# Kernel tuning notes

Measured on AMD Instinct MI355X. Metric: run time of the kernel, lower is better.

The kernel has to match this reference:

```python
import jax, jax.numpy as jnp
import numpy as np
from jax import lax

BN_EPS = 1e-5

def conv_bn_prelu(x, w, b, scale, bias, a):
    # Conv2d(k=3, pad=1, stride=1) in NCHW / OIHW layout
    y = lax.conv_general_dilated(x, w, window_strides=(1, 1), padding='SAME',
                                 dimension_numbers=('NCHW', 'OIHW', 'NCHW'))
    y = y + b[None, :, None, None]
    # BatchNorm2d, training-mode batch statistics over (B, H, W)
    mean = jnp.mean(y, axis=(0, 2, 3), keepdims=True)
    var = jnp.var(y, axis=(0, 2, 3), keepdims=True)
    y = (y - mean) * lax.rsqrt(var + BN_EPS)
    y = y * scale[None, :, None, None] + bias[None, :, None, None]
    # PReLU with single shared slope parameter
    return jnp.where(y >= 0, y, a * y)

def setup_inputs() -> dict:
    key = jax.random.key(0)
    ks = jax.random.split(key, 7)
    B, C, H, W = 4, 64, 64, 64
    x = jax.random.normal(ks[0], (B, C, H, W), dtype=jnp.float32)
    conv_w = jax.random.normal(ks[1], (C, C, 3, 3), dtype=jnp.float32) * 0.05
    conv_b = jax.random.normal(ks[2], (C,), dtype=jnp.float32) * 0.05
    bn_scale = jax.random.uniform(ks[3], (C,), dtype=jnp.float32, minval=0.5, maxval=1.5)
    bn_bias = jax.random.normal(ks[4], (C,), dtype=jnp.float32) * 0.05
    prelu_a = jnp.full((1,), 0.25, dtype=jnp.float32)
    gamma = jax.random.normal(ks[5], (1,), dtype=jnp.float32)
    return {'x': x, 'conv_w': conv_w, 'conv_b': conv_b, 'bn_scale': bn_scale,
            'bn_bias': bn_bias, 'prelu_a': prelu_a, 'gamma': gamma}

def reference(x, conv_w, conv_b, bn_scale, bn_bias, prelu_a, gamma):
    B, C, H, W = x.shape
    N = H * W
    feat = conv_bn_prelu(x, conv_w, conv_b, bn_scale, bn_bias, prelu_a)  # (B,C,H,W)
    f = feat.reshape(B, C, N)  # proj_query = f^T, proj_key = f, proj_value = f
    # energy[b,i,j] = sum_c f[b,c,i] * f[b,c,j]  -> (B, N, N)
    energy = jnp.einsum('bci,bcj->bij', f, f)
    # energy_new = rowmax - energy, softmax over last dim
    energy_new = jnp.max(energy, axis=-1, keepdims=True) - energy
    attn = jax.nn.softmax(energy_new, axis=-1)
    # out = bmm(proj_value, attention^T): out[b,c,i] = sum_j f[b,c,j] * attn[b,i,j]
    out = jnp.einsum('bcj,bij->bci', f, attn).reshape(B, C, H, W)
    return gamma * out + feat
```

## Files before the change

kernel.cpp:

```cpp
#include <hip/hip_runtime.h>

constexpr int kB = 4, kC = 64, kH = 64, kW = 64, kN = kH * kW;
constexpr float kEps = 1e-5f;
constexpr int SPLIT = 4;

typedef __attribute__((ext_vector_type(8))) short short8;
typedef __attribute__((ext_vector_type(4))) float f32x4;
typedef unsigned short u16;

__device__ inline unsigned pkbf(float a, float b) {
  unsigned ua = __float_as_uint(a), ub = __float_as_uint(b);
  ua += 0x7fff + ((ua >> 16) & 1);
  ub += 0x7fff + ((ub >> 16) & 1);
  return (ua >> 16) | (ub & 0xffff0000u);
}

__global__ __launch_bounds__(256) void prep_w_kernel(const float* __restrict__ w,
                                                     u16* __restrict__ wA) {
  int idx = blockIdx.x * 256 + threadIdx.x;
  if (idx < 64 * 576) {
    int oc = idx / 576, r = idx - oc * 576;
    int khw = r >> 6, ic = r & 63;
    float v = w[(oc * 64 + ic) * 9 + khw];
    unsigned u = __float_as_uint(v);
    u += 0x7fff + ((u >> 16) & 1);
    wA[idx] = (u16)(u >> 16);
  }
}

__global__ __launch_bounds__(256) void conv_kernel(const float* __restrict__ x,
                                                   const u16* __restrict__ wA,
                                                   const float* __restrict__ bias,
                                                   float* __restrict__ y) {
  const int tid = threadIdx.x;
  const int lane = tid & 63;
  const int wv = tid >> 6;
  const int bx = blockIdx.x;
  const int b = bx >> 7;
  const int h = (bx & 127) >> 1;
  const int w0 = (bx & 1) * 32;
  const int lw = lane & 15, lg = lane >> 4;

  __shared__ __align__(16) u16 xt[3 * 40 * 64];

#pragma unroll
  for (int rep = 0; rep < 4; ++rep) {
    int idx = rep * 256 + tid;
    if (idx < 960) {
      int kh = idx / 320;
      int t = idx - kh * 320;
      int gw = t >> 5, icp = t & 31;
      int wb = w0 - 4 + gw * 4;
      int hh = h + kh - 1;
      float4 va = {0.f, 0.f, 0.f, 0.f}, vb = {0.f, 0.f, 0.f, 0.f};
      if (hh >= 0 && hh < 64 && wb >= 0 && wb < 64) {
        va = *(const float4*)&x[((b * 64 + icp * 2) * 64 + hh) * 64 + wb];
        vb = *(const float4*)&x[((b * 64 + icp * 2 + 1) * 64 + hh) * 64 + wb];
      }
      float av[4] = {va.x, va.y, va.z, va.w};
      float bv[4] = {vb.x, vb.y, vb.z, vb.w};
#pragma unroll
      for (int j = 0; j < 4; ++j) {
        int wc = gw * 4 + j;
        *(unsigned*)&xt[(kh * 40 + wc) * 64 + (((icp >> 2) ^ (wc & 7)) * 8 + (icp & 3) * 2)] =
            pkbf(av[j], bv[j]);
      }
    }
  }
  __syncthreads();

  const int oc0 = wv * 16;
  short8 af[18];
#pragma unroll
  for (int kc = 0; kc < 18; ++kc)
    af[kc] = *(const short8*)&wA[(oc0 + lw) * 576 + kc * 32 + lg * 8];

  f32x4 acc[2];
  acc[0] = (f32x4){0.f, 0.f, 0.f, 0.f};
  acc[1] = (f32x4){0.f, 0.f, 0.f, 0.f};
#pragma unroll
  for (int kc = 0; kc < 18; ++kc) {
    const int khw = kc >> 1;
    const int kh = khw / 3, kwv = khw % 3;
#pragma unroll
    for (int nt = 0; nt < 2; ++nt) {
      int wc = nt * 16 + lw + kwv + 3;
      short8 bf = *(const short8*)&xt[(kh * 40 + wc) * 64 + ((((kc & 1) * 4 + lg) ^ (wc & 7)) * 8)];
      acc[nt] = __builtin_amdgcn_mfma_f32_16x16x32_bf16(af[kc], bf, acc[nt], 0, 0, 0);
    }
  }
#pragma unroll
  for (int nt = 0; nt < 2; ++nt)
#pragma unroll
    for (int r = 0; r < 4; ++r) {
      int oc = oc0 + lg * 4 + r;
      y[((b * 64 + oc) * 64 + h) * 64 + w0 + nt * 16 + lw] = acc[nt][r] + bias[oc];
    }
}

__global__ __launch_bounds__(256) void stats_kernel(const float* __restrict__ y,
                                                    const float* __restrict__ scale,
                                                    const float* __restrict__ bias,
                                                    float* __restrict__ AB) {
  const int c = blockIdx.x;
  const int tid = threadIdx.x;
  float s = 0.f, s2 = 0.f;
  for (int b = 0; b < kB; ++b) {
    const float* p = y + (b * kC + c) * kN;
    for (int i = tid * 4; i < kN; i += 1024) {
      float4 v = *(const float4*)(p + i);
      s += v.x + v.y + v.z + v.w;
      s2 += v.x * v.x + v.y * v.y + v.z * v.z + v.w * v.w;
    }
  }
  __shared__ float rs[256], rq[256];
  rs[tid] = s;
  rq[tid] = s2;
  __syncthreads();
  for (int off = 128; off > 0; off >>= 1) {
    if (tid < off) { rs[tid] += rs[tid + off]; rq[tid] += rq[tid + off]; }
    __syncthreads();
  }
  if (tid == 0) {
    const float inv_n = 1.f / (float)(kB * kN);
    float mean = rs[0] * inv_n;
    float var = rq[0] * inv_n - mean * mean;
    float A = scale[c] * rsqrtf(var + kEps);
    AB[c] = A;
    AB[kC + c] = bias[c] - mean * A;
  }
}

__global__ __launch_bounds__(256) void pack_kernel(const float* __restrict__ y,
                                                   const float* __restrict__ AB,
                                                   const float* __restrict__ pa,
                                                   float* __restrict__ feat,
                                                   u16* __restrict__ fbfA,
                                                   u16* __restrict__ fbfB) {
  __shared__ float ls[64 * 65];
  const int tid = threadIdx.x;
  const int b = blockIdx.x >> 6;
  const int n0 = (blockIdx.x & 63) << 6;
  {
    const int c = tid >> 2, nj = (tid & 3) << 4;
    const float A = AB[c], Bc = AB[kC + c], a = pa[0];
    const float* yp = y + ((b * kC + c) * kN) + n0 + nj;
    float f[16];
#pragma unroll
    for (int v = 0; v < 4; ++v) {
      float4 xv = *(const float4*)(yp + v * 4);
      float t;
      t = fmaf(A, xv.x, Bc); f[v * 4 + 0] = t >= 0.f ? t : a * t;
      t = fmaf(A, xv.y, Bc); f[v * 4 + 1] = t >= 0.f ? t : a * t;
      t = fmaf(A, xv.z, Bc); f[v * 4 + 2] = t >= 0.f ? t : a * t;
      t = fmaf(A, xv.w, Bc); f[v * 4 + 3] = t >= 0.f ? t : a * t;
    }
    float* fo = feat + ((b * kC + c) * kN) + n0 + nj;
#pragma unroll
    for (int v = 0; v < 4; ++v) {
      float4 fv = {f[v * 4 + 0], f[v * 4 + 1], f[v * 4 + 2], f[v * 4 + 3]};
      *(float4*)(fo + v * 4) = fv;
    }
#pragma unroll
    for (int v = 0; v < 16; ++v) ls[c * 65 + nj + v] = f[v];
  }
  __syncthreads();
  {
    int chunk = tid >> 5, pt = chunk >> 1, kc = chunk & 1;
    int lp2 = (tid & 31) * 2;
    u16* dst = fbfA + ((size_t)((b * 256 + (n0 >> 4) + pt) * 2 + kc)) * 512;
#pragma unroll
    for (int e = 0; e < 2; ++e) {
      int L = lp2 + e;
      int n = pt * 16 + (L & 15);
      int cb = kc * 32 + (L >> 4) * 8;
      float v[8];
#pragma unroll
      for (int r = 0; r < 8; ++r) v[r] = ls[(cb + r) * 65 + n];
      uint4 o = {pkbf(v[0], v[1]), pkbf(v[2], v[3]), pkbf(v[4], v[5]), pkbf(v[6], v[7])};
      *(uint4*)&dst[L * 8] = o;
    }
  }
  {
    int chunk = tid >> 5, jt = chunk >> 2, ct = chunk & 3;
    int lp2 = (tid & 31) * 2;
    u16* dst = fbfB + ((size_t)((b * 128 + (n0 >> 5) + jt) * 4 + ct)) * 512;
#pragma unroll
    for (int e = 0; e < 2; ++e) {
      int L = lp2 + e;
      int c = ct * 16 + (L & 15);
      int nb = jt * 32 + (L >> 4) * 8;
      float v[8];
#pragma unroll
      for (int r = 0; r < 8; ++r) v[r] = ls[c * 65 + nb + r];
      uint4 o = {pkbf(v[0], v[1]), pkbf(v[2], v[3]), pkbf(v[4], v[5]), pkbf(v[6], v[7])};
      *(uint4*)&dst[L * 8] = o;
    }
  }
}

__global__ __launch_bounds__(256, 2) void attn_kernel(const u16* __restrict__ fbfA,
                                                      const u16* __restrict__ fbfB,
                                                      float* __restrict__ Op,
                                                      float* __restrict__ lp) {
  const int tid = threadIdx.x;
  const int lane = tid & 63;
  const int w = tid >> 6;
  const int bx = blockIdx.x;
  const int s = bx & 3, itb = (bx >> 2) & 15, b = bx >> 6;
  const int c15 = lane & 15, g = lane >> 4;

  __shared__ __align__(16) u16 Ps[4][64 * 40];
  u16* ps = &Ps[w][0];
  const int pw_off = c15 * 40 + g * 4;
  const int pr_off = c15 * 40 + g * 8;

  const uint4* fA = (const uint4*)fbfA;
  const uint4* fB = (const uint4*)fbfB;

  uint4 qf[4][2];
  const int ptq = itb * 16 + w * 4;
#pragma unroll
  for (int it = 0; it < 4; ++it)
#pragma unroll
    for (int kc = 0; kc < 2; ++kc) {
      uint4 q = fA[(size_t)((b * 256 + ptq + it) * 2 + kc) * 64 + lane];
      q.x ^= 0x80008000u; q.y ^= 0x80008000u; q.z ^= 0x80008000u; q.w ^= 0x80008000u;
      qf[it][kc] = q;
    }

  const short8 ones = {0x3F80, 0x3F80, 0x3F80, 0x3F80, 0x3F80, 0x3F80, 0x3F80, 0x3F80};

  f32x4 oacc[4][4];
  f32x4 lacc[4];
#pragma unroll
  for (int it = 0; it < 4; ++it) {
    lacc[it] = (f32x4){0.f, 0.f, 0.f, 0.f};
#pragma unroll
    for (int ct = 0; ct < 4; ++ct) oacc[it][ct] = (f32x4){0.f, 0.f, 0.f, 0.f};
  }

#pragma unroll 2
  for (int jj = 0; jj < 32; ++jj) {
    const int j0 = (s * 32 + jj) * 32;
    const int ca = (b * 256 + (j0 >> 4)) * 2;
    uint4 a00 = fA[(size_t)(ca + 0) * 64 + lane];
    uint4 a01 = fA[(size_t)(ca + 1) * 64 + lane];
    uint4 a10 = fA[(size_t)(ca + 2) * 64 + lane];
    uint4 a11 = fA[(size_t)(ca + 3) * 64 + lane];
    const int cb = (b * 128 + (j0 >> 5)) * 4;
    uint4 v0 = fB[(size_t)(cb + 0) * 64 + lane];
    uint4 v1 = fB[(size_t)(cb + 1) * 64 + lane];
    uint4 v2 = fB[(size_t)(cb + 2) * 64 + lane];
    uint4 v3 = fB[(size_t)(cb + 3) * 64 + lane];

    f32x4 sv[2][4];
#pragma unroll
    for (int it = 0; it < 4; ++it) {
      f32x4 z0 = (f32x4){0.f, 0.f, 0.f, 0.f};
      z0 = __builtin_amdgcn_mfma_f32_16x16x32_bf16(*(short8*)&a00, *(short8*)&qf[it][0], z0, 0, 0, 0);
      z0 = __builtin_amdgcn_mfma_f32_16x16x32_bf16(*(short8*)&a01, *(short8*)&qf[it][1], z0, 0, 0, 0);
      sv[0][it] = z0;
      f32x4 z1 = (f32x4){0.f, 0.f, 0.f, 0.f};
      z1 = __builtin_amdgcn_mfma_f32_16x16x32_bf16(*(short8*)&a10, *(short8*)&qf[it][0], z1, 0, 0, 0);
      z1 = __builtin_amdgcn_mfma_f32_16x16x32_bf16(*(short8*)&a11, *(short8*)&qf[it][1], z1, 0, 0, 0);
      sv[1][it] = z1;
    }
#pragma unroll
    for (int it = 0; it < 4; ++it)
#pragma unroll
      for (int jt = 0; jt < 2; ++jt) {
        float p0 = __expf(sv[jt][it][0]);
        float p1 = __expf(sv[jt][it][1]);
        float p2 = __expf(sv[jt][it][2]);
        float p3 = __expf(sv[jt][it][3]);
        uint2 d;
        d.x = __builtin_amdgcn_perm(__float_as_uint(p1), __float_as_uint(p0), 0x07060302u);
        d.y = __builtin_amdgcn_perm(__float_as_uint(p3), __float_as_uint(p2), 0x07060302u);
        *(uint2*)&ps[pw_off + it * 640 + jt * 16] = d;
      }
#pragma unroll
    for (int it = 0; it < 4; ++it) {
      short8 pf = *(const short8*)&ps[pr_off + it * 640];
      lacc[it] = __builtin_amdgcn_mfma_f32_16x16x32_bf16(pf, ones, lacc[it], 0, 0, 0);
      oacc[it][0] = __builtin_amdgcn_mfma_f32_16x16x32_bf16(pf, *(short8*)&v0, oacc[it][0], 0, 0, 0);
      oacc[it][1] = __builtin_amdgcn_mfma_f32_16x16x32_bf16(pf, *(short8*)&v1, oacc[it][1], 0, 0, 0);
      oacc[it][2] = __builtin_amdgcn_mfma_f32_16x16x32_bf16(pf, *(short8*)&v2, oacc[it][2], 0, 0, 0);
      oacc[it][3] = __builtin_amdgcn_mfma_f32_16x16x32_bf16(pf, *(short8*)&v3, oacc[it][3], 0, 0, 0);
    }
  }

  float* Ow = Op + (size_t)(bx * 4 + w) * 4096;
#pragma unroll
  for (int it = 0; it < 4; ++it)
#pragma unroll
    for (int ct = 0; ct < 4; ++ct)
#pragma unroll
      for (int r = 0; r < 4; ++r)
        Ow[(it * 16 + g * 4 + r) * 64 + ct * 16 + c15] = oacc[it][ct][r];
  if (c15 == 0) {
    float* lw_ = lp + (size_t)(bx * 4 + w) * 64;
#pragma unroll
    for (int it = 0; it < 4; ++it)
#pragma unroll
      for (int r = 0; r < 4; ++r) lw_[it * 16 + g * 4 + r] = lacc[it][r];
  }
}

__global__ __launch_bounds__(256) void combine_kernel(const float* __restrict__ Op,
                                                      const float* __restrict__ lp,
                                                      const float* __restrict__ feat,
                                                      const float* __restrict__ gamma_p,
                                                      float* __restrict__ out) {
  const int tid = threadIdx.x;
  const int bx = blockIdx.x;
  const int b = bx >> 6, it64 = bx & 63;
  const int itb = it64 >> 2, w = it64 & 3;
  const int gbase = (b * 16 + itb) * 16 + w;
  __shared__ float tr[64 * 65];
  __shared__ float linv[64];
  if (tid < 64) {
    float sum = 0.f;
    for (int s = 0; s < SPLIT; ++s) sum += lp[(size_t)(gbase + s * 4) * 64 + tid];
    linv[tid] = 1.f / sum;
  }
  __syncthreads();
  const float gm = gamma_p[0];
#pragma unroll
  for (int rr = 0; rr < 4; ++rr) {
    int flat4 = rr * 256 + tid;
    int i = flat4 >> 4, c4 = (flat4 & 15) * 4;
    float4 acc = {0.f, 0.f, 0.f, 0.f};
    for (int s = 0; s < SPLIT; ++s) {
      float4 v = *(const float4*)&Op[(size_t)(gbase + s * 4) * 4096 + i * 64 + c4];
      acc.x += v.x; acc.y += v.y; acc.z += v.z; acc.w += v.w;
    }
    float sc = gm * linv[i];
    tr[(c4 + 0) * 65 + i] = acc.x * sc;
    tr[(c4 + 1) * 65 + i] = acc.y * sc;
    tr[(c4 + 2) * 65 + i] = acc.z * sc;
    tr[(c4 + 3) * 65 + i] = acc.w * sc;
  }
  __syncthreads();
#pragma unroll
  for (int rr = 0; rr < 4; ++rr) {
    int flat4 = rr * 256 + tid;
    int c = flat4 >> 4, i4 = (flat4 & 15) * 4;
    float4 fv = *(const float4*)&feat[(size_t)(b * 64 + c) * 4096 + it64 * 64 + i4];
    float4 ov;
    ov.x = tr[c * 65 + i4 + 0] + fv.x;
    ov.y = tr[c * 65 + i4 + 1] + fv.y;
    ov.z = tr[c * 65 + i4 + 2] + fv.z;
    ov.w = tr[c * 65 + i4 + 3] + fv.w;
    *(float4*)&out[(size_t)(b * 64 + c) * 4096 + it64 * 64 + i4] = ov;
  }
}

extern "C" void kernel_launch(void* const* d_in, const int* in_sizes, int n_in,
                              void* d_out, int out_size, void* d_ws, size_t ws_size,
                              hipStream_t stream) {
  (void)in_sizes; (void)n_in; (void)out_size; (void)ws_size;
  const float* x        = (const float*)d_in[0];
  const float* conv_w   = (const float*)d_in[1];
  const float* conv_b   = (const float*)d_in[2];
  const float* bn_scale = (const float*)d_in[3];
  const float* bn_bias  = (const float*)d_in[4];
  const float* prelu_a  = (const float*)d_in[5];
  const float* gamma    = (const float*)d_in[6];
  float* out = (float*)d_out;

  float* feat = (float*)d_ws;
  u16* fbfA = (u16*)(feat + kB * kC * kN);
  u16* fbfB = fbfA + kB * kC * kN;
  float* AB = (float*)(fbfB + kB * kC * kN);
  u16* wA = (u16*)(AB + 256);
  float* Op = (float*)(wA + 36864);
  float* lp = Op + (size_t)256 * 4 * 4096;

  float* y = out;

  prep_w_kernel<<<144, 256, 0, stream>>>(conv_w, wA);
  conv_kernel<<<kB * kH * 2, 256, 0, stream>>>(x, wA, conv_b, y);
  stats_kernel<<<kC, 256, 0, stream>>>(y, bn_scale, bn_bias, AB);
  pack_kernel<<<kB * (kN / 64), 256, 0, stream>>>(y, AB, prelu_a, feat, fbfA, fbfB);
  attn_kernel<<<kB * 16 * SPLIT, 256, 0, stream>>>(fbfA, fbfB, Op, lp);
  combine_kernel<<<kB * 64, 256, 0, stream>>>(Op, lp, feat, gamma, out);
}
```

Baseline: 123.3 us.

## Fuse BN stats into conv, drop feat buffer, exp2 softmax, smaller attention tiles

Batch-norm sums are now accumulated inside the conv kernel with wave shuffles and atomics, which removes the separate stats kernel. The feat tensor is no longer written; combine recomputes the BN+PReLU from y. The query operand is pre-scaled by log2(e) so the softmax can use the hardware exp2. The attention grid is doubled with half as many query rows per block, and the partial output layout is rearranged. The trade-offs are atomic contention on the stats, order-dependent float summation, and some extra recompute in combine.

```diff
diff --git a/kernel.cpp b/kernel.cpp
--- a/kernel.cpp
+++ b/kernel.cpp
@@ -3,6 +3,13 @@
 constexpr int kB = 4, kC = 64, kH = 64, kW = 64, kN = kH * kW;
 constexpr float kEps = 1e-5f;
 constexpr int SPLIT = 4;
+constexpr float kQS = 1.2011224087864498f;
+
+#if __has_builtin(__builtin_amdgcn_exp2f)
+#define EXP2F(x) __builtin_amdgcn_exp2f(x)
+#else
+#define EXP2F(x) exp2f(x)
+#endif
 
 typedef __attribute__((ext_vector_type(8))) short short8;
 typedef __attribute__((ext_vector_type(4))) float f32x4;
@@ -16,7 +23,12 @@
 }
 
 __global__ __launch_bounds__(256) void prep_w_kernel(const float* __restrict__ w,
-                                                     u16* __restrict__ wA) {
+                                                     u16* __restrict__ wA,
+                                                     float* __restrict__ stat) {
+  if (blockIdx.x == 0) {
+    stat[threadIdx.x] = 0.f;
+    stat[256 + threadIdx.x] = 0.f;
+  }
   int idx = blockIdx.x * 256 + threadIdx.x;
   if (idx < 64 * 576) {
     int oc = idx / 576, r = idx - oc * 576;
@@ -31,7 +43,8 @@
 __global__ __launch_bounds__(256) void conv_kernel(const float* __restrict__ x,
                                                    const u16* __restrict__ wA,
                                                    const float* __restrict__ bias,
-                                                   float* __restrict__ y) {
+                                                   float* __restrict__ y,
+                                                   float* __restrict__ stat) {
   const int tid = threadIdx.x;
   const int lane = tid & 63;
   const int wv = tid >> 6;
@@ -89,61 +102,59 @@
       acc[nt] = __builtin_amdgcn_mfma_f32_16x16x32_bf16(af[kc], bf, acc[nt], 0, 0, 0);
     }
   }
-#pragma unroll
-  for (int nt = 0; nt < 2; ++nt)
-#pragma unroll
-    for (int r = 0; r < 4; ++r) {
-      int oc = oc0 + lg * 4 + r;
-      y[((b * 64 + oc) * 64 + h) * 64 + w0 + nt * 16 + lw] = acc[nt][r] + bias[oc];
-    }
-}
-
-__global__ __launch_bounds__(256) void stats_kernel(const float* __restrict__ y,
-                                                    const float* __restrict__ scale,
-                                                    const float* __restrict__ bias,
-                                                    float* __restrict__ AB) {
-  const int c = blockIdx.x;
-  const int tid = threadIdx.x;
-  float s = 0.f, s2 = 0.f;
-  for (int b = 0; b < kB; ++b) {
-    const float* p = y + (b * kC + c) * kN;
-    for (int i = tid * 4; i < kN; i += 1024) {
-      float4 v = *(const float4*)(p + i);
-      s += v.x + v.y + v.z + v.w;
-      s2 += v.x * v.x + v.y * v.y + v.z * v.z + v.w * v.w;
-    }
-  }
-  __shared__ float rs[256], rq[256];
-  rs[tid] = s;
-  rq[tid] = s2;
-  __syncthreads();
-  for (int off = 128; off > 0; off >>= 1) {
-    if (tid < off) { rs[tid] += rs[tid + off]; rq[tid] += rq[tid + off]; }
-    __syncthreads();
-  }
-  if (tid == 0) {
-    const float inv_n = 1.f / (float)(kB * kN);
-    float mean = rs[0] * inv_n;
-    float var = rq[0] * inv_n - mean * mean;
-    float A = scale[c] * rsqrtf(var + kEps);
-    AB[c] = A;
-    AB[kC + c] = bias[c] - mean * A;
+
+  float* st = stat + (bx & 3) * 128;
+#pragma unroll
+  for (int r = 0; r < 4; ++r) {
+    const int oc = oc0 + lg * 4 + r;
+    const float bz = bias[oc];
+    float v0 = acc[0][r] + bz;
+    float v1 = acc[1][r] + bz;
+    y[((b * 64 + oc) * 64 + h) * 64 + w0 + lw] = v0;
+    y[((b * 64 + oc) * 64 + h) * 64 + w0 + 16 + lw] = v1;
+    float s = v0 + v1, q = v0 * v0 + v1 * v1;
+#pragma unroll
+    for (int m = 1; m < 16; m <<= 1) {
+      s += __shfl_xor(s, m);
+      q += __shfl_xor(q, m);
+    }
+    if (lw == 0) {
+      atomicAdd(&st[oc], s);
+      atomicAdd(&st[64 + oc], q);
+    }
   }
 }
 
 __global__ __launch_bounds__(256) void pack_kernel(const float* __restrict__ y,
-                                                   const float* __restrict__ AB,
+                                                   const float* __restrict__ stat,
+                                                   const float* __restrict__ scale,
+                                                   const float* __restrict__ bias,
                                                    const float* __restrict__ pa,
-                                                   float* __restrict__ feat,
+                                                   float* __restrict__ ABg,
                                                    u16* __restrict__ fbfA,
                                                    u16* __restrict__ fbfB) {
   __shared__ float ls[64 * 65];
+  __shared__ float sAB[128];
   const int tid = threadIdx.x;
   const int b = blockIdx.x >> 6;
   const int n0 = (blockIdx.x & 63) << 6;
+  if (tid < 64) {
+    const float inv_n = 1.f / (float)(kB * kN);
+    float ssum = stat[tid] + stat[128 + tid] + stat[256 + tid] + stat[384 + tid];
+    float qsum = stat[64 + tid] + stat[192 + tid] + stat[320 + tid] + stat[448 + tid];
+    float mean = ssum * inv_n;
+    float var = qsum * inv_n - mean * mean;
+    float A = scale[tid] * rsqrtf(var + kEps);
+    float Bc = bias[tid] - mean * A;
+    sAB[tid] = A;
+    sAB[64 + tid] = Bc;
+    ABg[tid] = A;
+    ABg[64 + tid] = Bc;
+  }
+  __syncthreads();
   {
     const int c = tid >> 2, nj = (tid & 3) << 4;
-    const float A = AB[c], Bc = AB[kC + c], a = pa[0];
+    const float A = sAB[c], Bc = sAB[64 + c], a = pa[0];
     const float* yp = y + ((b * kC + c) * kN) + n0 + nj;
     float f[16];
 #pragma unroll
@@ -155,12 +166,6 @@
       t = fmaf(A, xv.z, Bc); f[v * 4 + 2] = t >= 0.f ? t : a * t;
       t = fmaf(A, xv.w, Bc); f[v * 4 + 3] = t >= 0.f ? t : a * t;
     }
-    float* fo = feat + ((b * kC + c) * kN) + n0 + nj;
-#pragma unroll
-    for (int v = 0; v < 4; ++v) {
-      float4 fv = {f[v * 4 + 0], f[v * 4 + 1], f[v * 4 + 2], f[v * 4 + 3]};
-      *(float4*)(fo + v * 4) = fv;
-    }
 #pragma unroll
     for (int v = 0; v < 16; ++v) ls[c * 65 + nj + v] = f[v];
   }
@@ -176,7 +181,7 @@
       int cb = kc * 32 + (L >> 4) * 8;
       float v[8];
 #pragma unroll
-      for (int r = 0; r < 8; ++r) v[r] = ls[(cb + r) * 65 + n];
+      for (int r = 0; r < 8; ++r) v[r] = kQS * ls[(cb + r) * 65 + n];
       uint4 o = {pkbf(v[0], v[1]), pkbf(v[2], v[3]), pkbf(v[4], v[5]), pkbf(v[6], v[7])};
       *(uint4*)&dst[L * 8] = o;
     }
@@ -207,10 +212,10 @@
   const int lane = tid & 63;
   const int w = tid >> 6;
   const int bx = blockIdx.x;
-  const int s = bx & 3, itb = (bx >> 2) & 15, b = bx >> 6;
+  const int s = bx & 3, itb = (bx >> 2) & 31, b = bx >> 7;
   const int c15 = lane & 15, g = lane >> 4;
 
-  __shared__ __align__(16) u16 Ps[4][64 * 40];
+  __shared__ __align__(16) u16 Ps[4][32 * 40];
   u16* ps = &Ps[w][0];
   const int pw_off = c15 * 40 + g * 4;
   const int pr_off = c15 * 40 + g * 8;
@@ -218,10 +223,10 @@
   const uint4* fA = (const uint4*)fbfA;
   const uint4* fB = (const uint4*)fbfB;
 
-  uint4 qf[4][2];
-  const int ptq = itb * 16 + w * 4;
-#pragma unroll
-  for (int it = 0; it < 4; ++it)
+  uint4 qf[2][2];
+  const int ptq = itb * 8 + w * 2;
+#pragma unroll
+  for (int it = 0; it < 2; ++it)
 #pragma unroll
     for (int kc = 0; kc < 2; ++kc) {
       uint4 q = fA[(size_t)((b * 256 + ptq + it) * 2 + kc) * 64 + lane];
@@ -231,10 +236,10 @@
 
   const short8 ones = {0x3F80, 0x3F80, 0x3F80, 0x3F80, 0x3F80, 0x3F80, 0x3F80, 0x3F80};
 
-  f32x4 oacc[4][4];
-  f32x4 lacc[4];
-#pragma unroll
-  for (int it = 0; it < 4; ++it) {
+  f32x4 oacc[2][4];
+  f32x4 lacc[2];
+#pragma unroll
+  for (int it = 0; it < 2; ++it) {
     lacc[it] = (f32x4){0.f, 0.f, 0.f, 0.f};
 #pragma unroll
     for (int ct = 0; ct < 4; ++ct) oacc[it][ct] = (f32x4){0.f, 0.f, 0.f, 0.f};
@@ -254,9 +259,9 @@
     uint4 v2 = fB[(size_t)(cb + 2) * 64 + lane];
     uint4 v3 = fB[(size_t)(cb + 3) * 64 + lane];
 
-    f32x4 sv[2][4];
-#pragma unroll
-    for (int it = 0; it < 4; ++it) {
+    f32x4 sv[2][2];
+#pragma unroll
+    for (int it = 0; it < 2; ++it) {
       f32x4 z0 = (f32x4){0.f, 0.f, 0.f, 0.f};
       z0 = __builtin_amdgcn_mfma_f32_16x16x32_bf16(*(short8*)&a00, *(short8*)&qf[it][0], z0, 0, 0, 0);
       z0 = __builtin_amdgcn_mfma_f32_16x16x32_bf16(*(short8*)&a01, *(short8*)&qf[it][1], z0, 0, 0, 0);
@@ -267,20 +272,20 @@
       sv[1][it] = z1;
     }
 #pragma unroll
-    for (int it = 0; it < 4; ++it)
+    for (int it = 0; it < 2; ++it)
 #pragma unroll
       for (int jt = 0; jt < 2; ++jt) {
-        float p0 = __expf(sv[jt][it][0]);
-        float p1 = __expf(sv[jt][it][1]);
-        float p2 = __expf(sv[jt][it][2]);
-        float p3 = __expf(sv[jt][it][3]);
+        float p0 = EXP2F(sv[jt][it][0]);
+        float p1 = EXP2F(sv[jt][it][1]);
+        float p2 = EXP2F(sv[jt][it][2]);
+        float p3 = EXP2F(sv[jt][it][3]);
         uint2 d;
         d.x = __builtin_amdgcn_perm(__float_as_uint(p1), __float_as_uint(p0), 0x07060302u);
         d.y = __builtin_amdgcn_perm(__float_as_uint(p3), __float_as_uint(p2), 0x07060302u);
         *(uint2*)&ps[pw_off + it * 640 + jt * 16] = d;
       }
 #pragma unroll
-    for (int it = 0; it < 4; ++it) {
+    for (int it = 0; it < 2; ++it) {
       short8 pf = *(const short8*)&ps[pr_off + it * 640];
       lacc[it] = __builtin_amdgcn_mfma_f32_16x16x32_bf16(pf, ones, lacc[it], 0, 0, 0);
       oacc[it][0] = __builtin_amdgcn_mfma_f32_16x16x32_bf16(pf, *(short8*)&v0, oacc[it][0], 0, 0, 0);
@@ -290,18 +295,19 @@
     }
   }
 
-  float* Ow = Op + (size_t)(bx * 4 + w) * 4096;
-#pragma unroll
-  for (int it = 0; it < 4; ++it)
+  const int rbase = (s * kB + b) * kN + itb * 128 + w * 32;
+  float* Ow = Op + (size_t)rbase * 64;
+#pragma unroll
+  for (int it = 0; it < 2; ++it)
 #pragma unroll
     for (int ct = 0; ct < 4; ++ct)
 #pragma unroll
       for (int r = 0; r < 4; ++r)
         Ow[(it * 16 + g * 4 + r) * 64 + ct * 16 + c15] = oacc[it][ct][r];
   if (c15 == 0) {
-    float* lw_ = lp + (size_t)(bx * 4 + w) * 64;
-#pragma unroll
-    for (int it = 0; it < 4; ++it)
+    float* lw_ = lp + rbase;
+#pragma unroll
+    for (int it = 0; it < 2; ++it)
 #pragma unroll
       for (int r = 0; r < 4; ++r) lw_[it * 16 + g * 4 + r] = lacc[it][r];
   }
@@ -309,30 +315,32 @@
 
 __global__ __launch_bounds__(256) void combine_kernel(const float* __restrict__ Op,
                                                       const float* __restrict__ lp,
-                                                      const float* __restrict__ feat,
+                                                      const float* __restrict__ y,
+                                                      const float* __restrict__ ABg,
+                                                      const float* __restrict__ pa,
                                                       const float* __restrict__ gamma_p,
                                                       float* __restrict__ out) {
   const int tid = threadIdx.x;
   const int bx = blockIdx.x;
   const int b = bx >> 6, it64 = bx & 63;
-  const int itb = it64 >> 2, w = it64 & 3;
-  const int gbase = (b * 16 + itb) * 16 + w;
+  const int i0 = it64 * 64;
   __shared__ float tr[64 * 65];
   __shared__ float linv[64];
   if (tid < 64) {
     float sum = 0.f;
-    for (int s = 0; s < SPLIT; ++s) sum += lp[(size_t)(gbase + s * 4) * 64 + tid];
+    for (int s = 0; s < SPLIT; ++s) sum += lp[(size_t)(s * kB + b) * kN + i0 + tid];
     linv[tid] = 1.f / sum;
   }
   __syncthreads();
   const float gm = gamma_p[0];
+  const float a = pa[0];
 #pragma unroll
   for (int rr = 0; rr < 4; ++rr) {
     int flat4 = rr * 256 + tid;
     int i = flat4 >> 4, c4 = (flat4 & 15) * 4;
     float4 acc = {0.f, 0.f, 0.f, 0.f};
     for (int s = 0; s < SPLIT; ++s) {
-      float4 v = *(const float4*)&Op[(size_t)(gbase + s * 4) * 4096 + i * 64 + c4];
+      float4 v = *(const float4*)&Op[((size_t)(s * kB + b) * kN + i0 + i) * 64 + c4];
       acc.x += v.x; acc.y += v.y; acc.z += v.z; acc.w += v.w;
     }
     float sc = gm * linv[i];
@@ -346,12 +354,14 @@
   for (int rr = 0; rr < 4; ++rr) {
     int flat4 = rr * 256 + tid;
     int c = flat4 >> 4, i4 = (flat4 & 15) * 4;
-    float4 fv = *(const float4*)&feat[(size_t)(b * 64 + c) * 4096 + it64 * 64 + i4];
+    const float A = ABg[c], Bc = ABg[64 + c];
+    float4 yv = *(const float4*)&y[(size_t)(b * 64 + c) * 4096 + it64 * 64 + i4];
+    float t;
     float4 ov;
-    ov.x = tr[c * 65 + i4 + 0] + fv.x;
-    ov.y = tr[c * 65 + i4 + 1] + fv.y;
-    ov.z = tr[c * 65 + i4 + 2] + fv.z;
-    ov.w = tr[c * 65 + i4 + 3] + fv.w;
+    t = fmaf(A, yv.x, Bc); t = t >= 0.f ? t : a * t; ov.x = tr[c * 65 + i4 + 0] + t;
+    t = fmaf(A, yv.y, Bc); t = t >= 0.f ? t : a * t; ov.y = tr[c * 65 + i4 + 1] + t;
+    t = fmaf(A, yv.z, Bc); t = t >= 0.f ? t : a * t; ov.z = tr[c * 65 + i4 + 2] + t;
+    t = fmaf(A, yv.w, Bc); t = t >= 0.f ? t : a * t; ov.w = tr[c * 65 + i4 + 3] + t;
     *(float4*)&out[(size_t)(b * 64 + c) * 4096 + it64 * 64 + i4] = ov;
   }
 }
@@ -369,20 +379,20 @@
   const float* gamma    = (const float*)d_in[6];
   float* out = (float*)d_out;
 
-  float* feat = (float*)d_ws;
-  u16* fbfA = (u16*)(feat + kB * kC * kN);
+  u16* fbfA = (u16*)d_ws;
   u16* fbfB = fbfA + kB * kC * kN;
-  float* AB = (float*)(fbfB + kB * kC * kN);
-  u16* wA = (u16*)(AB + 256);
+  float* stat = (float*)(fbfB + kB * kC * kN);
+  float* ABg = stat + 512;
+  u16* wA = (u16*)(ABg + 128);
   float* Op = (float*)(wA + 36864);
-  float* lp = Op + (size_t)256 * 4 * 4096;
+  float* lp = Op + (size_t)16 * kN * 64;
 
   float* y = out;
 
-  prep_w_kernel<<<144, 256, 0, stream>>>(conv_w, wA);
-  conv_kernel<<<kB * kH * 2, 256, 0, stream>>>(x, wA, conv_b, y);
-  stats_kernel<<<kC, 256, 0, stream>>>(y, bn_scale, bn_bias, AB);
-  pack_kernel<<<kB * (kN / 64), 256, 0, stream>>>(y, AB, prelu_a, feat, fbfA, fbfB);
-  attn_kernel<<<kB * 16 * SPLIT, 256, 0, stream>>>(fbfA, fbfB, Op, lp);
-  combine_kernel<<<kB * 64, 256, 0, stream>>>(Op, lp, feat, gamma, out);
-}
+  prep_w_kernel<<<144, 256, 0, stream>>>(conv_w, wA, stat);
+  conv_kernel<<<kB * kH * 2, 256, 0, stream>>>(x, wA, conv_b, y, stat);
+  pack_kernel<<<kB * (kN / 64), 256, 0, stream>>>(y, stat, bn_scale, bn_bias, prelu_a,
+                                                  ABg, fbfA, fbfB);
+  attn_kernel<<<kB * 32 * SPLIT, 256, 0, stream>>>(fbfA, fbfB, Op, lp);
+  combine_kernel<<<kB * 64, 256, 0, stream>>>(Op, lp, y, ABg, prelu_a, gamma, out);
+}
```

After: 132.7 us. 7.7% more time.
